# Performance work log

Measured on AMD Instinct MI355X. Metric: run time of the kernel, lower is better.

Reference implementation:

```python
import jax, jax.numpy as jnp
import numpy as np

N_NODES = 50000
N_EDGES = 800000
IN_CH = 64
HID_CH = 128
OUT_CH = 64
N_GRAPHS = 512


def setup_inputs() -> dict:
    key = jax.random.key(0)
    ks = jax.random.split(key, 10)
    x = jax.random.normal(ks[0], (N_NODES, IN_CH), dtype=jnp.float32)
    edge_index = jax.random.randint(ks[1], (2, N_EDGES), 0, N_NODES, dtype=jnp.int64)
    batch = jnp.sort(jax.random.randint(ks[2], (N_NODES,), 0, N_GRAPHS, dtype=jnp.int64))
    s = 1.0 / np.sqrt(IN_CH)
    # SAGEConv (mean aggr): lin_l applied to aggregated neighbors (with bias),
    # lin_r applied to root features (no bias).
    W_l = jax.random.uniform(ks[3], (HID_CH, IN_CH), minval=-s, maxval=s, dtype=jnp.float32)
    b_l = jax.random.uniform(ks[4], (HID_CH,), minval=-s, maxval=s, dtype=jnp.float32)
    W_r = jax.random.uniform(ks[5], (HID_CH, IN_CH), minval=-s, maxval=s, dtype=jnp.float32)
    sh = 1.0 / np.sqrt(HID_CH)
    W_att = jax.random.uniform(ks[6], (1, HID_CH), minval=-sh, maxval=sh, dtype=jnp.float32)
    b_att = jax.random.uniform(ks[7], (1,), minval=-sh, maxval=sh, dtype=jnp.float32)
    W_out = jax.random.uniform(ks[8], (OUT_CH, HID_CH), minval=-sh, maxval=sh, dtype=jnp.float32)
    b_out = jax.random.uniform(ks[9], (OUT_CH,), minval=-sh, maxval=sh, dtype=jnp.float32)
    return {"x": x, "edge_index": edge_index, "batch": batch,
            "W_l": W_l, "b_l": b_l, "W_r": W_r,
            "W_att": W_att, "b_att": b_att, "W_out": W_out, "b_out": b_out}


def reference(x, edge_index, batch, W_l, b_l, W_r, W_att, b_att, W_out, b_out):
    src, dst = edge_index[0], edge_index[1]
    # mean aggregation of neighbor (source) features at each target node
    agg = jax.ops.segment_sum(x[src], dst, num_segments=N_NODES)  # [N, IN]
    deg = jax.ops.segment_sum(jnp.ones((N_EDGES,), x.dtype), dst, num_segments=N_NODES)
    agg = agg / jnp.maximum(deg, 1.0)[:, None]
    # SAGEConv: lin_l(aggr) + lin_r(x), then ReLU
    h = jax.nn.relu(agg @ W_l.T + b_l + x @ W_r.T)  # [N, HID]
    # attention weighting
    scores = jax.nn.sigmoid(h @ W_att.T + b_att)  # [N, 1]
    h = h * scores
    # global mean pool per graph
    pooled = jax.ops.segment_sum(h, batch, num_segments=N_GRAPHS)  # [B, HID]
    counts = jax.ops.segment_sum(jnp.ones((N_NODES,), x.dtype), batch, num_segments=N_GRAPHS)
    pooled = pooled / jnp.maximum(counts, 1.0)[:, None]
    return pooled @ W_out.T + b_out  # [B, OUT]
```

## Files before the change

### kernel.cpp

```cpp
#include <hip/hip_runtime.h>
#include <hip/hip_bf16.h>

#define N_NODES 50000
#define N_EDGES 800000
#define IN_CH 64
#define HID_CH 128
#define OUT_CH 64
#define N_GRAPHS 512
#define CAP 64
#define TN 16
#define NPB 128
#define NSTAGE (NPB / TN)

typedef unsigned short ushort_t;
typedef unsigned int uint_t;

__device__ __forceinline__ void atomAddF(float* p, float v) {
    unsafeAtomicAdd(p, v);
}

__device__ __forceinline__ ushort_t f2bf(float f) {
    uint_t b = __float_as_uint(f);
    return (ushort_t)((b + 0x7fffu + ((b >> 16) & 1u)) >> 16);
}


__global__ __launch_bounds__(256) void convert_x(
    const float* __restrict__ x, ushort_t* __restrict__ xh)
{
    int i = blockIdx.x * 256 + threadIdx.x;
    if (i >= N_NODES * IN_CH / 8) return;
    const float4 f0 = *reinterpret_cast<const float4*>(x + (size_t)i * 8);
    const float4 f1 = *reinterpret_cast<const float4*>(x + (size_t)i * 8 + 4);
    uint4 o;
    o.x = (uint_t)f2bf(f0.x) | ((uint_t)f2bf(f0.y) << 16);
    o.y = (uint_t)f2bf(f0.z) | ((uint_t)f2bf(f0.w) << 16);
    o.z = (uint_t)f2bf(f1.x) | ((uint_t)f2bf(f1.y) << 16);
    o.w = (uint_t)f2bf(f1.z) | ((uint_t)f2bf(f1.w) << 16);
    *reinterpret_cast<uint4*>(xh + (size_t)i * 8) = o;
}

__global__ __launch_bounds__(256) void scatter_pad(
    const int* __restrict__ ei, int* __restrict__ degi,
    ushort_t* __restrict__ csr16)
{
    int e = blockIdx.x * 256 + threadIdx.x;
    if (e >= N_EDGES) return;
    int src = ei[e];
    int dst = ei[N_EDGES + e];
    int pos = atomicAdd(&degi[dst], 1);
    csr16[(dst << 6) + pos] = (ushort_t)src;
}

__global__ __launch_bounds__(256) void gather_bf16(
    const ushort_t* __restrict__ xh, const ushort_t* __restrict__ csr16,
    const int* __restrict__ degi, float* __restrict__ agg)
{
    int wid  = (blockIdx.x * 256 + threadIdx.x) >> 6;
    int lane = threadIdx.x & 63;
    if (wid >= N_NODES) return;
    int d = degi[wid];
    const ushort_t* b = csr16 + ((size_t)wid << 6);
    int g  = lane >> 3;
    int c8 = lane & 7;
    float a0[8] = {0.f, 0.f, 0.f, 0.f, 0.f, 0.f, 0.f, 0.f};
    float a1[8] = {0.f, 0.f, 0.f, 0.f, 0.f, 0.f, 0.f, 0.f};
    int i = g;
    for (; i + 8 < d; i += 16) {
        int s0 = b[i], s1 = b[i + 8];
        uint4 u0 = *reinterpret_cast<const uint4*>(xh + (size_t)s0 * IN_CH + c8 * 8);
        uint4 u1 = *reinterpret_cast<const uint4*>(xh + (size_t)s1 * IN_CH + c8 * 8);
        a0[0] += __uint_as_float(u0.x << 16); a0[1] += __uint_as_float(u0.x & 0xffff0000u);
        a0[2] += __uint_as_float(u0.y << 16); a0[3] += __uint_as_float(u0.y & 0xffff0000u);
        a0[4] += __uint_as_float(u0.z << 16); a0[5] += __uint_as_float(u0.z & 0xffff0000u);
        a0[6] += __uint_as_float(u0.w << 16); a0[7] += __uint_as_float(u0.w & 0xffff0000u);
        a1[0] += __uint_as_float(u1.x << 16); a1[1] += __uint_as_float(u1.x & 0xffff0000u);
        a1[2] += __uint_as_float(u1.y << 16); a1[3] += __uint_as_float(u1.y & 0xffff0000u);
        a1[4] += __uint_as_float(u1.z << 16); a1[5] += __uint_as_float(u1.z & 0xffff0000u);
        a1[6] += __uint_as_float(u1.w << 16); a1[7] += __uint_as_float(u1.w & 0xffff0000u);
    }
    if (i < d) {
        int s0 = b[i];
        uint4 u0 = *reinterpret_cast<const uint4*>(xh + (size_t)s0 * IN_CH + c8 * 8);
        a0[0] += __uint_as_float(u0.x << 16); a0[1] += __uint_as_float(u0.x & 0xffff0000u);
        a0[2] += __uint_as_float(u0.y << 16); a0[3] += __uint_as_float(u0.y & 0xffff0000u);
        a0[4] += __uint_as_float(u0.z << 16); a0[5] += __uint_as_float(u0.z & 0xffff0000u);
        a0[6] += __uint_as_float(u0.w << 16); a0[7] += __uint_as_float(u0.w & 0xffff0000u);
    }
#pragma unroll
    for (int k = 0; k < 8; ++k) {
        a0[k] += a1[k];
        a0[k] += __shfl_xor(a0[k], 8);
        a0[k] += __shfl_xor(a0[k], 16);
        a0[k] += __shfl_xor(a0[k], 32);
    }
    if (g == 0) {
        float inv = 1.0f / fmaxf((float)d, 1.0f);
        float4 w0 = make_float4(a0[0] * inv, a0[1] * inv, a0[2] * inv, a0[3] * inv);
        float4 w1 = make_float4(a0[4] * inv, a0[5] * inv, a0[6] * inv, a0[7] * inv);
        *reinterpret_cast<float4*>(agg + (size_t)wid * IN_CH + c8 * 8)     = w0;
        *reinterpret_cast<float4*>(agg + (size_t)wid * IN_CH + c8 * 8 + 4) = w1;
    }
}

__global__ __launch_bounds__(256, 4) void node_kernel(
    const float* __restrict__ x, const float* __restrict__ agg,
    const int* __restrict__ batch,
    const float* __restrict__ Wl, const float* __restrict__ bl,
    const float* __restrict__ Wr, const float* __restrict__ Watt,
    const float* __restrict__ batt,
    float* __restrict__ pooled, float* __restrict__ counts)
{
    const int t    = threadIdx.x;
    const int jp   = t & 63;
    const int q    = t >> 6;
    const int lane = t & 63;

    float4 wl0[4], wl1[4], wr0[4], wr1[4];
#pragma unroll
    for (int c = 0; c < 4; ++c) {
        wl0[c] = *reinterpret_cast<const float4*>(Wl + (size_t)jp * IN_CH + q * 16 + c * 4);
        wr0[c] = *reinterpret_cast<const float4*>(Wr + (size_t)jp * IN_CH + q * 16 + c * 4);
        wl1[c] = *reinterpret_cast<const float4*>(Wl + (size_t)(jp + 64) * IN_CH + q * 16 + c * 4);
        wr1[c] = *reinterpret_cast<const float4*>(Wr + (size_t)(jp + 64) * IN_CH + q * 16 + c * 4);
    }
    const int jj    = t & 127;
    const float blj = bl[jj];
    const float wa  = Watt[jj];
    const float ba  = batt[0];

    __shared__ __align__(16) float4 feat[TN][32];
    float* sh = reinterpret_cast<float*>(feat);
    __shared__ float psum[4][TN][HID_CH];
    __shared__ float sred[2][TN];
    __shared__ float ss[TN];

    float accp = 0.f, cnt = 0.f;
    const int nb0 = blockIdx.x * NPB;
    int curb = batch[nb0];

    for (int s = 0; s < NSTAGE; ++s) {
        const int nb = nb0 + s * TN;
        if (nb >= N_NODES) break;
        __syncthreads();
#pragma unroll
        for (int k = 0; k < 2; ++k) {
            int f    = t + k * 256;
            int node = nb + (f >> 5);
            int slot = f & 31;
            const float* src = (slot < 16)
                ? x   + (size_t)node * IN_CH + slot * 4
                : agg + (size_t)node * IN_CH + (slot - 16) * 4;
            feat[f >> 5][slot] = *reinterpret_cast<const float4*>(src);
        }
        __syncthreads();

#pragma unroll
        for (int n = 0; n < TN; ++n) {
            float p0a = 0.f, p0b = 0.f, p1a = 0.f, p1b = 0.f;
#pragma unroll
            for (int c = 0; c < 4; ++c) {
                float4 xv = feat[n][q * 4 + c];
                float4 av = feat[n][16 + q * 4 + c];
                p0a += wr0[c].x * xv.x + wr0[c].y * xv.y
                     + wl0[c].x * av.x + wl0[c].y * av.y;
                p0b += wr0[c].z * xv.z + wr0[c].w * xv.w
                     + wl0[c].z * av.z + wl0[c].w * av.w;
                p1a += wr1[c].x * xv.x + wr1[c].y * xv.y
                     + wl1[c].x * av.x + wl1[c].y * av.y;
                p1b += wr1[c].z * xv.z + wr1[c].w * xv.w
                     + wl1[c].z * av.z + wl1[c].w * av.w;
            }
            psum[q][n][jp]      = p0a + p0b;
            psum[q][n][jp + 64] = p1a + p1b;
        }
        __syncthreads();

        if (t < 128) {
#pragma unroll
            for (int n = 0; n < TN; ++n) {
                float h = psum[0][n][jj] + psum[1][n][jj]
                        + psum[2][n][jj] + psum[3][n][jj] + blj;
                h = fmaxf(h, 0.f);
                sh[n * HID_CH + jj] = h;
                float r = wa * h;
                r += __shfl_xor(r, 1);  r += __shfl_xor(r, 2);
                r += __shfl_xor(r, 4);  r += __shfl_xor(r, 8);
                r += __shfl_xor(r, 16); r += __shfl_xor(r, 32);
                if (lane == n) sred[t >> 6][n] = r;
            }
        }
        __syncthreads();
        if (t < TN) ss[t] = 1.f / (1.f + expf(-(sred[0][t] + sred[1][t] + ba)));
        __syncthreads();

        if (t < 128) {
#pragma unroll
            for (int n = 0; n < TN; ++n) {
                float hs = sh[n * HID_CH + jj] * ss[n];
                int b = batch[nb + n];
                if (b != curb) {
                    atomAddF(&pooled[(size_t)curb * HID_CH + jj], accp);
                    if (jj == 0) atomAddF(&counts[curb], cnt);
                    accp = 0.f; cnt = 0.f; curb = b;
                }
                accp += hs;
                cnt  += 1.f;
            }
        }
    }
    if (t < 128) {
        atomAddF(&pooled[(size_t)curb * HID_CH + jj], accp);
        if (jj == 0) atomAddF(&counts[curb], cnt);
    }
}

__global__ __launch_bounds__(64) void out_kernel(
    const float* __restrict__ pooled, const float* __restrict__ counts,
    const float* __restrict__ Wout, const float* __restrict__ bout,
    float* __restrict__ out)
{
    const int g = blockIdx.x;
    const int j = threadIdx.x;
    __shared__ __align__(16) float sp[HID_CH];
    float inv = 1.0f / fmaxf(counts[g], 1.0f);
    sp[j]      = pooled[(size_t)g * HID_CH + j] * inv;
    sp[j + 64] = pooled[(size_t)g * HID_CH + 64 + j] * inv;
    __syncthreads();
    float acc = bout[j];
#pragma unroll
    for (int c4 = 0; c4 < HID_CH / 4; ++c4) {
        float4 w = *reinterpret_cast<const float4*>(Wout + (size_t)j * HID_CH + c4 * 4);
        acc += w.x * sp[c4 * 4 + 0] + w.y * sp[c4 * 4 + 1]
             + w.z * sp[c4 * 4 + 2] + w.w * sp[c4 * 4 + 3];
    }
    out[(size_t)g * OUT_CH + j] = acc;
}

extern "C" void kernel_launch(void* const* d_in, const int* in_sizes, int n_in,
                              void* d_out, int out_size, void* d_ws, size_t ws_size,
                              hipStream_t stream)
{
    const float* x     = (const float*)d_in[0];
    const int*   ei    = (const int*)d_in[1];
    const int*   batch = (const int*)d_in[2];
    const float* Wl    = (const float*)d_in[3];
    const float* bl    = (const float*)d_in[4];
    const float* Wr    = (const float*)d_in[5];
    const float* Watt  = (const float*)d_in[6];
    const float* batt  = (const float*)d_in[7];
    const float* Wout  = (const float*)d_in[8];
    const float* bout  = (const float*)d_in[9];
    float* out = (float*)d_out;

    int*      degi   = (int*)d_ws;
    float*    pooled = (float*)(degi + N_NODES);
    float*    counts = pooled + (size_t)N_GRAPHS * HID_CH;
    ushort_t* csr16  = (ushort_t*)(counts + N_GRAPHS);
    float*    agg    = (float*)(csr16 + (size_t)N_NODES * CAP);
    ushort_t* xh     = (ushort_t*)(agg + (size_t)N_NODES * IN_CH);

    size_t zero_bytes = ((size_t)N_NODES
                       + (size_t)N_GRAPHS * HID_CH + N_GRAPHS) * sizeof(int);
    hipMemsetAsync(d_ws, 0, zero_bytes, stream);

    convert_x<<<(N_NODES * IN_CH / 8 + 255) / 256, 256, 0, stream>>>(x, xh);
    scatter_pad<<<(N_EDGES + 255) / 256, 256, 0, stream>>>(ei, degi, csr16);
    gather_bf16<<<(N_NODES * 64 + 255) / 256, 256, 0, stream>>>(xh, csr16, degi, agg);
    node_kernel<<<(N_NODES + NPB - 1) / NPB, 256, 0, stream>>>(
        x, agg, batch, Wl, bl, Wr, Watt, batt, pooled, counts);
    out_kernel<<<N_GRAPHS, 64, 0, stream>>>(pooled, counts, Wout, bout, out);
}
```

Measured before the change: 244.3 us.

## Fuse neighbor gather into node kernel and fold memset into convert kernel

Moves the bf16 neighbor mean-aggregation into the node kernel, where each wavefront aggregates four nodes straight into shared memory. This removes the separate gather launch and the fp32 agg buffer's write and read. The workspace memset is also replaced by zeroing inside convert_x, and NPB is halved so there are enough blocks for the work that now sits in node_kernel. In exchange, node_kernel now carries the latency-bound irregular gather, and its occupancy limit (launch bounds 256,4) may hide that latency less well than the standalone gather kernel did.

```diff
diff --git a/kernel.cpp b/kernel.cpp
--- a/kernel.cpp
+++ b/kernel.cpp
@@ -9,7 +9,7 @@
 #define N_GRAPHS 512
 #define CAP 64
 #define TN 16
-#define NPB 128
+#define NPB 64
 #define NSTAGE (NPB / TN)
 
 typedef unsigned short ushort_t;
@@ -24,11 +24,15 @@
     return (ushort_t)((b + 0x7fffu + ((b >> 16) & 1u)) >> 16);
 }
 
-
 __global__ __launch_bounds__(256) void convert_x(
-    const float* __restrict__ x, ushort_t* __restrict__ xh)
+    const float* __restrict__ x, ushort_t* __restrict__ xh,
+    int* __restrict__ degi, float* __restrict__ pooled,
+    float* __restrict__ counts)
 {
     int i = blockIdx.x * 256 + threadIdx.x;
+    if (i < N_NODES) degi[i] = 0;
+    if (i < N_GRAPHS * HID_CH) pooled[i] = 0.f;
+    if (i < N_GRAPHS) counts[i] = 0.f;
     if (i >= N_NODES * IN_CH / 8) return;
     const float4 f0 = *reinterpret_cast<const float4*>(x + (size_t)i * 8);
     const float4 f1 = *reinterpret_cast<const float4*>(x + (size_t)i * 8 + 4);
@@ -52,59 +56,9 @@
     csr16[(dst << 6) + pos] = (ushort_t)src;
 }
 
-__global__ __launch_bounds__(256) void gather_bf16(
-    const ushort_t* __restrict__ xh, const ushort_t* __restrict__ csr16,
-    const int* __restrict__ degi, float* __restrict__ agg)
-{
-    int wid  = (blockIdx.x * 256 + threadIdx.x) >> 6;
-    int lane = threadIdx.x & 63;
-    if (wid >= N_NODES) return;
-    int d = degi[wid];
-    const ushort_t* b = csr16 + ((size_t)wid << 6);
-    int g  = lane >> 3;
-    int c8 = lane & 7;
-    float a0[8] = {0.f, 0.f, 0.f, 0.f, 0.f, 0.f, 0.f, 0.f};
-    float a1[8] = {0.f, 0.f, 0.f, 0.f, 0.f, 0.f, 0.f, 0.f};
-    int i = g;
-    for (; i + 8 < d; i += 16) {
-        int s0 = b[i], s1 = b[i + 8];
-        uint4 u0 = *reinterpret_cast<const uint4*>(xh + (size_t)s0 * IN_CH + c8 * 8);
-        uint4 u1 = *reinterpret_cast<const uint4*>(xh + (size_t)s1 * IN_CH + c8 * 8);
-        a0[0] += __uint_as_float(u0.x << 16); a0[1] += __uint_as_float(u0.x & 0xffff0000u);
-        a0[2] += __uint_as_float(u0.y << 16); a0[3] += __uint_as_float(u0.y & 0xffff0000u);
-        a0[4] += __uint_as_float(u0.z << 16); a0[5] += __uint_as_float(u0.z & 0xffff0000u);
-        a0[6] += __uint_as_float(u0.w << 16); a0[7] += __uint_as_float(u0.w & 0xffff0000u);
-        a1[0] += __uint_as_float(u1.x << 16); a1[1] += __uint_as_float(u1.x & 0xffff0000u);
-        a1[2] += __uint_as_float(u1.y << 16); a1[3] += __uint_as_float(u1.y & 0xffff0000u);
-        a1[4] += __uint_as_float(u1.z << 16); a1[5] += __uint_as_float(u1.z & 0xffff0000u);
-        a1[6] += __uint_as_float(u1.w << 16); a1[7] += __uint_as_float(u1.w & 0xffff0000u);
-    }
-    if (i < d) {
-        int s0 = b[i];
-        uint4 u0 = *reinterpret_cast<const uint4*>(xh + (size_t)s0 * IN_CH + c8 * 8);
-        a0[0] += __uint_as_float(u0.x << 16); a0[1] += __uint_as_float(u0.x & 0xffff0000u);
-        a0[2] += __uint_as_float(u0.y << 16); a0[3] += __uint_as_float(u0.y & 0xffff0000u);
-        a0[4] += __uint_as_float(u0.z << 16); a0[5] += __uint_as_float(u0.z & 0xffff0000u);
-        a0[6] += __uint_as_float(u0.w << 16); a0[7] += __uint_as_float(u0.w & 0xffff0000u);
-    }
-#pragma unroll
-    for (int k = 0; k < 8; ++k) {
-        a0[k] += a1[k];
-        a0[k] += __shfl_xor(a0[k], 8);
-        a0[k] += __shfl_xor(a0[k], 16);
-        a0[k] += __shfl_xor(a0[k], 32);
-    }
-    if (g == 0) {
-        float inv = 1.0f / fmaxf((float)d, 1.0f);
-        float4 w0 = make_float4(a0[0] * inv, a0[1] * inv, a0[2] * inv, a0[3] * inv);
-        float4 w1 = make_float4(a0[4] * inv, a0[5] * inv, a0[6] * inv, a0[7] * inv);
-        *reinterpret_cast<float4*>(agg + (size_t)wid * IN_CH + c8 * 8)     = w0;
-        *reinterpret_cast<float4*>(agg + (size_t)wid * IN_CH + c8 * 8 + 4) = w1;
-    }
-}
-
 __global__ __launch_bounds__(256, 4) void node_kernel(
-    const float* __restrict__ x, const float* __restrict__ agg,
+    const float* __restrict__ x, const ushort_t* __restrict__ xh,
+    const ushort_t* __restrict__ csr16, const int* __restrict__ degi,
     const int* __restrict__ batch,
     const float* __restrict__ Wl, const float* __restrict__ bl,
     const float* __restrict__ Wr, const float* __restrict__ Watt,
@@ -115,6 +69,8 @@
     const int jp   = t & 63;
     const int q    = t >> 6;
     const int lane = t & 63;
+    const int g8   = lane >> 3;
+    const int c8   = lane & 7;
 
     float4 wl0[4], wl1[4], wr0[4], wr1[4];
 #pragma unroll
@@ -143,15 +99,56 @@
         const int nb = nb0 + s * TN;
         if (nb >= N_NODES) break;
         __syncthreads();
-#pragma unroll
-        for (int k = 0; k < 2; ++k) {
-            int f    = t + k * 256;
-            int node = nb + (f >> 5);
-            int slot = f & 31;
-            const float* src = (slot < 16)
-                ? x   + (size_t)node * IN_CH + slot * 4
-                : agg + (size_t)node * IN_CH + (slot - 16) * 4;
-            feat[f >> 5][slot] = *reinterpret_cast<const float4*>(src);
+
+        {
+            int node = t >> 4, slot = t & 15;
+            feat[node][slot] = *reinterpret_cast<const float4*>(
+                x + (size_t)(nb + node) * IN_CH + slot * 4);
+        }
+#pragma unroll
+        for (int u = 0; u < 4; ++u) {
+            const int n    = (q << 2) | u;
+            const int node = nb + n;
+            const int d    = degi[node];
+            const ushort_t* b = csr16 + ((size_t)node << 6);
+            float a0[8] = {0.f,0.f,0.f,0.f,0.f,0.f,0.f,0.f};
+            float a1[8] = {0.f,0.f,0.f,0.f,0.f,0.f,0.f,0.f};
+            int i = g8;
+            for (; i + 8 < d; i += 16) {
+                int s0 = b[i], s1 = b[i + 8];
+                uint4 u0 = *reinterpret_cast<const uint4*>(xh + (size_t)s0 * IN_CH + c8 * 8);
+                uint4 u1 = *reinterpret_cast<const uint4*>(xh + (size_t)s1 * IN_CH + c8 * 8);
+                a0[0] += __uint_as_float(u0.x << 16); a0[1] += __uint_as_float(u0.x & 0xffff0000u);
+                a0[2] += __uint_as_float(u0.y << 16); a0[3] += __uint_as_float(u0.y & 0xffff0000u);
+                a0[4] += __uint_as_float(u0.z << 16); a0[5] += __uint_as_float(u0.z & 0xffff0000u);
+                a0[6] += __uint_as_float(u0.w << 16); a0[7] += __uint_as_float(u0.w & 0xffff0000u);
+                a1[0] += __uint_as_float(u1.x << 16); a1[1] += __uint_as_float(u1.x & 0xffff0000u);
+                a1[2] += __uint_as_float(u1.y << 16); a1[3] += __uint_as_float(u1.y & 0xffff0000u);
+                a1[4] += __uint_as_float(u1.z << 16); a1[5] += __uint_as_float(u1.z & 0xffff0000u);
+                a1[6] += __uint_as_float(u1.w << 16); a1[7] += __uint_as_float(u1.w & 0xffff0000u);
+            }
+            if (i < d) {
+                int s0 = b[i];
+                uint4 u0 = *reinterpret_cast<const uint4*>(xh + (size_t)s0 * IN_CH + c8 * 8);
+                a0[0] += __uint_as_float(u0.x << 16); a0[1] += __uint_as_float(u0.x & 0xffff0000u);
+                a0[2] += __uint_as_float(u0.y << 16); a0[3] += __uint_as_float(u0.y & 0xffff0000u);
+                a0[4] += __uint_as_float(u0.z << 16); a0[5] += __uint_as_float(u0.z & 0xffff0000u);
+                a0[6] += __uint_as_float(u0.w << 16); a0[7] += __uint_as_float(u0.w & 0xffff0000u);
+            }
+#pragma unroll
+            for (int k = 0; k < 8; ++k) {
+                a0[k] += a1[k];
+                a0[k] += __shfl_xor(a0[k], 8);
+                a0[k] += __shfl_xor(a0[k], 16);
+                a0[k] += __shfl_xor(a0[k], 32);
+            }
+            if (g8 == 0) {
+                float inv = 1.0f / fmaxf((float)d, 1.0f);
+                feat[n][16 + 2 * c8] = make_float4(a0[0] * inv, a0[1] * inv,
+                                                   a0[2] * inv, a0[3] * inv);
+                feat[n][17 + 2 * c8] = make_float4(a0[4] * inv, a0[5] * inv,
+                                                   a0[6] * inv, a0[7] * inv);
+            }
         }
         __syncthreads();
 
@@ -257,17 +254,12 @@
     float*    pooled = (float*)(degi + N_NODES);
     float*    counts = pooled + (size_t)N_GRAPHS * HID_CH;
     ushort_t* csr16  = (ushort_t*)(counts + N_GRAPHS);
-    float*    agg    = (float*)(csr16 + (size_t)N_NODES * CAP);
-    ushort_t* xh     = (ushort_t*)(agg + (size_t)N_NODES * IN_CH);
-
-    size_t zero_bytes = ((size_t)N_NODES
-                       + (size_t)N_GRAPHS * HID_CH + N_GRAPHS) * sizeof(int);
-    hipMemsetAsync(d_ws, 0, zero_bytes, stream);
-
-    convert_x<<<(N_NODES * IN_CH / 8 + 255) / 256, 256, 0, stream>>>(x, xh);
+    ushort_t* xh     = csr16 + (size_t)N_NODES * CAP;
+
+    convert_x<<<(N_NODES * IN_CH / 8 + 255) / 256, 256, 0, stream>>>(
+        x, xh, degi, pooled, counts);
     scatter_pad<<<(N_EDGES + 255) / 256, 256, 0, stream>>>(ei, degi, csr16);
-    gather_bf16<<<(N_NODES * 64 + 255) / 256, 256, 0, stream>>>(xh, csr16, degi, agg);
     node_kernel<<<(N_NODES + NPB - 1) / NPB, 256, 0, stream>>>(
-        x, agg, batch, Wl, bl, Wr, Watt, batt, pooled, counts);
+        x, xh, csr16, degi, batch, Wl, bl, Wr, Watt, batt, pooled, counts);
     out_kernel<<<N_GRAPHS, 64, 0, stream>>>(pooled, counts, Wout, bout, out);
 }
```

New measurement: 269.1 us. 1.1x slower.
